# Performance work log

Hardware: AMD Instinct MI355X
Metric: run time of the kernel (lower is better)

## Reference

```python
import jax, jax.numpy as jnp
import numpy as np

B, L, D = 1, 1024, 128
EPS = 1e-5


def setup_inputs() -> dict:
    key = jax.random.key(0)
    ks = jax.random.split(key, 10)
    s = 1.0 / np.sqrt(D)
    return {
        "x": jax.random.normal(ks[0], (B, L, D), dtype=jnp.float32),
        "mask": jax.random.randint(ks[1], (B, L, L), 0, 2, dtype=jnp.int32),
        # JCrossOutProduct.l : Linear(D, D)
        "Wl": jax.random.uniform(ks[2], (D, D), jnp.float32, -s, s),
        "bl": jax.random.uniform(ks[3], (D,), jnp.float32, -s, s),
        # JCrossOutProduct.lo : Linear(D, D)
        "Wlo": jax.random.uniform(ks[4], (D, D), jnp.float32, -s, s),
        "blo": jax.random.uniform(ks[5], (D,), jnp.float32, -s, s),
        # JResCOPAttn.l : Linear(D, D)
        "Wl2": jax.random.uniform(ks[6], (D, D), jnp.float32, -s, s),
        "bl2": jax.random.uniform(ks[7], (D,), jnp.float32, -s, s),
        # LayerNorm(D)
        "gamma": jnp.ones((D,), jnp.float32),
        "beta": jnp.zeros((D,), jnp.float32),
    }


def reference(x, mask, Wl, bl, Wlo, blo, Wl2, bl2, gamma, beta):
    # a = self.cop.l(x) : [B, L, D]
    a = x @ Wl.T + bl
    # outer product kept per-channel: [B, L, L, D]
    outer = jnp.einsum('blc,bmc->blmc', a, a)
    # self.cop.lo over last dim: [B, L, L, D]
    tm = outer @ Wlo.T + blo
    # masked_fill(mask.unsqueeze(-1) == 0, 0.0)
    tm = tm * (mask[..., None] != 0).astype(tm.dtype)
    # tx = self.l(x)
    tx = x @ Wl2.T + bl2
    # per-channel attention-like contraction: out[b,c,d] = sum_a tm[b,c,a,d] * tx[b,a,d]
    y = x + jnp.einsum('bcad,bad->bcd', tm, tx)
    # shadow (eval): Dropout=identity, activator 'none'=identity, LayerNorm(D)
    mu = jnp.mean(y, axis=-1, keepdims=True)
    var = jnp.mean(jnp.square(y - mu), axis=-1, keepdims=True)
    return (y - mu) * jax.lax.rsqrt(var + EPS) * gamma + beta
```

## Files before the change

### kernel.cpp

```cpp
#include <hip/hip_runtime.h>
#include <hip/hip_fp16.h>


typedef _Float16 f16x8 __attribute__((ext_vector_type(8)));
typedef float    f32x4 __attribute__((ext_vector_type(4)));
typedef unsigned int       u32;
typedef unsigned long long u64;

#define LL   1024
#define DD   128
#define EPSV 1e-5f

__global__ __launch_bounds__(256) void prep_kernel(
    const float* __restrict__ x,  const float* __restrict__ Wl,
    const float* __restrict__ bl, const float* __restrict__ Wlo,
    const float* __restrict__ Wl2,const float* __restrict__ bl2,
    _Float16* __restrict__ a_h, float* __restrict__ tx_out,
    _Float16* __restrict__ wh)
{
    __shared__ float xs[16*128];
    __shared__ float wsh[64*129];
    const int t  = threadIdx.x;
    const int bx = blockIdx.x;
    const int by = blockIdx.y;
    const int l0 = by*16;

    #pragma unroll
    for (int i = 0; i < 8; ++i) { int f = i*256 + t; xs[f] = x[l0*DD + f]; }
    const float* Wsrc = ((bx < 2) ? Wl : Wl2) + (bx & 1)*64*DD;
    #pragma unroll
    for (int i = 0; i < 32; ++i) {
        int f = i*256 + t; int r = f >> 7, k = f & 127;
        wsh[r*129 + k] = Wsrc[f];
    }
    __syncthreads();

    const int col  = t & 63;
    const int lsub = t >> 6;
    const float4* X4 = (const float4*)xs;
    float acc0 = 0.f, acc1 = 0.f, acc2 = 0.f, acc3 = 0.f;
    #pragma unroll
    for (int k4 = 0; k4 < 32; ++k4) {
        const float* wp = wsh + col*129 + k4*4;
        float4 wv = {wp[0], wp[1], wp[2], wp[3]};
        float4 x0 = X4[(lsub*4+0)*32 + k4];
        float4 x1 = X4[(lsub*4+1)*32 + k4];
        float4 x2 = X4[(lsub*4+2)*32 + k4];
        float4 x3 = X4[(lsub*4+3)*32 + k4];
        acc0 += wv.x*x0.x + wv.y*x0.y + wv.z*x0.z + wv.w*x0.w;
        acc1 += wv.x*x1.x + wv.y*x1.y + wv.z*x1.z + wv.w*x1.w;
        acc2 += wv.x*x2.x + wv.y*x2.y + wv.z*x2.z + wv.w*x2.w;
        acc3 += wv.x*x3.x + wv.y*x3.y + wv.z*x3.z + wv.w*x3.w;
    }
    const int colg = (bx & 1)*64 + col;
    const float bv = ((bx < 2) ? bl : bl2)[colg];
    if (bx < 2) {
        a_h[(l0+lsub*4+0)*DD + colg] = (_Float16)(acc0 + bv);
        a_h[(l0+lsub*4+1)*DD + colg] = (_Float16)(acc1 + bv);
        a_h[(l0+lsub*4+2)*DD + colg] = (_Float16)(acc2 + bv);
        a_h[(l0+lsub*4+3)*DD + colg] = (_Float16)(acc3 + bv);
    } else {
        tx_out[(l0+lsub*4+0)*DD + colg] = acc0 + bv;
        tx_out[(l0+lsub*4+1)*DD + colg] = acc1 + bv;
        tx_out[(l0+lsub*4+2)*DD + colg] = acc2 + bv;
        tx_out[(l0+lsub*4+3)*DD + colg] = acc3 + bv;
    }

    const int gid = (by*4 + bx)*256 + t;
    if (gid < DD*DD) wh[gid] = (_Float16)Wlo[gid];
}

#define COMPUTE(MI, AM, TV)                                                   \
  do {                                                                        \
    f16x8 ah_[4];                                                             \
    _Pragma("unroll")                                                         \
    for (int k_ = 0; k_ < 4; ++k_) ah_[k_] = al[k_] * (AM)[k_];               \
    f32x4 c_[4];                                                              \
    _Pragma("unroll")                                                         \
    for (int nf_ = 0; nf_ < 4; ++nf_)                                         \
      c_[nf_] = f32x4{blov[nf_], blov[nf_], blov[nf_], blov[nf_]};            \
    _Pragma("unroll")                                                         \
    for (int k_ = 0; k_ < 4; ++k_) {                                          \
      c_[0] = __builtin_amdgcn_mfma_f32_16x16x32_f16(ah_[k_], bh[0][k_], c_[0],0,0,0); \
      c_[1] = __builtin_amdgcn_mfma_f32_16x16x32_f16(ah_[k_], bh[1][k_], c_[1],0,0,0); \
      c_[2] = __builtin_amdgcn_mfma_f32_16x16x32_f16(ah_[k_], bh[2][k_], c_[2],0,0,0); \
      c_[3] = __builtin_amdgcn_mfma_f32_16x16x32_f16(ah_[k_], bh[3][k_], c_[3],0,0,0); \
    }                                                                         \
    _Pragma("unroll")                                                         \
    for (int r_ = 0; r_ < 4; ++r_) {                                          \
      const bool on_ = ((wmb[r_] >> (MI)) & 1ull) != 0;                       \
      _Pragma("unroll")                                                       \
      for (int nf_ = 0; nf_ < 4; ++nf_)                                       \
        y[nf_][r_] = fmaf(on_ ? (TV)[nf_] : 0.0f, c_[nf_][r_], y[nf_][r_]);   \
    }                                                                         \
  } while (0)

__global__ __launch_bounds__(256, 2) void heavy_kernel(
    const _Float16* __restrict__ a_h, const float* __restrict__ tx,
    const _Float16* __restrict__ wh,  const int* __restrict__ mask,
    const float* __restrict__ blo,    float* __restrict__ part)
{
    __shared__ __align__(16) _Float16 ash[64*DD];
    __shared__ __align__(4)  _Float16 txt[DD*66];
    __shared__ u64 mbits[32];
    const int t     = threadIdx.x;
    const int lane  = t & 63, w = t >> 6;
    const int chunk = blockIdx.x;
    const int ltile = blockIdx.y;
    const int l0 = ltile*32, m0 = chunk*64;

    {
        const float4* s4 = (const float4*)(a_h + m0*DD);
        float4* d4 = (float4*)ash;
        #pragma unroll
        for (int i = 0; i < 4; ++i) d4[i*256 + t] = s4[i*256 + t];
    }
    {
        #pragma unroll
        for (int i = 0; i < 8; ++i) {
            int idx = i*256 + t;
            int m = idx >> 5, dg = idx & 31;
            float4 v = *(const float4*)(tx + (m0+m)*DD + dg*4);
            txt[(dg*4+0)*66 + m] = (_Float16)v.x;
            txt[(dg*4+1)*66 + m] = (_Float16)v.y;
            txt[(dg*4+2)*66 + m] = (_Float16)v.z;
            txt[(dg*4+3)*66 + m] = (_Float16)v.w;
        }
    }
    {
        #pragma unroll
        for (int i = 0; i < 8; ++i) {
            int idx = i*256 + t;
            int row = idx >> 6, mcol = idx & 63;
            u64 b = __ballot(mask[(l0 + row)*LL + m0 + mcol] != 0);
            if ((t & 63) == 0) mbits[row] = b;
        }
    }
    __syncthreads();

    const int grp = lane >> 4, ln = lane & 15;
    const int wl = w >> 1, wd = w & 1;
    const int lbase = l0 + wl*16;
    const int dbase = wd*64;

    f16x8 bh[4][4];
    #pragma unroll
    for (int nf = 0; nf < 4; ++nf)
        #pragma unroll
        for (int k = 0; k < 4; ++k)
            bh[nf][k] = *(const f16x8*)(wh + (dbase + nf*16 + ln)*DD + k*32 + grp*8);

    f16x8 al[4];
    #pragma unroll
    for (int k = 0; k < 4; ++k)
        al[k] = *(const f16x8*)(a_h + (lbase + ln)*DD + k*32 + grp*8);

    float blov[4];
    #pragma unroll
    for (int nf = 0; nf < 4; ++nf) blov[nf] = blo[dbase + nf*16 + ln];

    const int lrow0 = wl*16 + grp*4;
    u64 wmb[4];
    #pragma unroll
    for (int r = 0; r < 4; ++r) wmb[r] = mbits[lrow0 + r];

    f32x4 y[4] = {{0,0,0,0},{0,0,0,0},{0,0,0,0},{0,0,0,0}};

    f16x8 amA[4], amB[4];
    float tvA[4], tvB[4], tvC[4], tvD[4];
    #pragma unroll
    for (int k = 0; k < 4; ++k)
        amA[k] = *(const f16x8*)(ash + 0*DD + k*32 + grp*8);
    #pragma unroll
    for (int nf = 0; nf < 4; ++nf) {
        float2 f2 = __half22float2(*(const __half2*)(txt + (dbase + nf*16 + ln)*66));
        tvA[nf] = f2.x; tvB[nf] = f2.y;
    }

    for (int ms = 0; ms < 62; ms += 2) {
        #pragma unroll
        for (int k = 0; k < 4; ++k)
            amB[k] = *(const f16x8*)(ash + (ms+1)*DD + k*32 + grp*8);
        #pragma unroll
        for (int nf = 0; nf < 4; ++nf) {
            float2 f2 = __half22float2(
                *(const __half2*)(txt + (dbase + nf*16 + ln)*66 + ms + 2));
            tvC[nf] = f2.x; tvD[nf] = f2.y;
        }
        COMPUTE(ms, amA, tvA);
        #pragma unroll
        for (int k = 0; k < 4; ++k)
            amA[k] = *(const f16x8*)(ash + (ms+2)*DD + k*32 + grp*8);
        COMPUTE(ms+1, amB, tvB);
        #pragma unroll
        for (int nf = 0; nf < 4; ++nf) { tvA[nf] = tvC[nf]; tvB[nf] = tvD[nf]; }
    }
    {
        #pragma unroll
        for (int k = 0; k < 4; ++k)
            amB[k] = *(const f16x8*)(ash + 63*DD + k*32 + grp*8);
        COMPUTE(62, amA, tvA);
        COMPUTE(63, amB, tvB);
    }

    float* dst = part + (size_t)chunk*(LL*DD);
    const int mrow0 = lbase + grp*4;
    #pragma unroll
    for (int nf = 0; nf < 4; ++nf)
        #pragma unroll
        for (int r = 0; r < 4; ++r)
            dst[(mrow0 + r)*DD + dbase + nf*16 + ln] = y[nf][r];
}

__global__ __launch_bounds__(128) void finish_kernel(
    const float* __restrict__ x, const float* __restrict__ part,
    const float* __restrict__ gamma, const float* __restrict__ beta,
    float* __restrict__ out)
{
    const int l = blockIdx.x, t = threadIdx.x;
    float v = x[l*DD + t];
    #pragma unroll
    for (int ch = 0; ch < 16; ++ch)
        v += part[((size_t)ch*LL + l)*DD + t];

    float s = v, s2 = v*v;
    #pragma unroll
    for (int o = 32; o > 0; o >>= 1) {
        s  += __shfl_xor(s, o);
        s2 += __shfl_xor(s2, o);
    }
    __shared__ float red[4];
    if ((t & 63) == 0) { red[(t>>6)*2+0] = s; red[(t>>6)*2+1] = s2; }
    __syncthreads();
    const float S  = red[0] + red[2];
    const float S2 = red[1] + red[3];
    const float mu  = S * (1.0f/128.0f);
    const float var = S2 * (1.0f/128.0f) - mu*mu;
    const float inv = rsqrtf(var + EPSV);
    out[l*DD + t] = (v - mu)*inv*gamma[t] + beta[t];
}

extern "C" void kernel_launch(void* const* d_in, const int* in_sizes, int n_in,
                              void* d_out, int out_size, void* d_ws, size_t ws_size,
                              hipStream_t stream)
{
    (void)in_sizes; (void)n_in; (void)out_size; (void)ws_size;
    const float* x     = (const float*)d_in[0];
    const int*   mask  = (const int*)  d_in[1];
    const float* Wl    = (const float*)d_in[2];
    const float* bl    = (const float*)d_in[3];
    const float* Wlo   = (const float*)d_in[4];
    const float* blo   = (const float*)d_in[5];
    const float* Wl2   = (const float*)d_in[6];
    const float* bl2   = (const float*)d_in[7];
    const float* gamma = (const float*)d_in[8];
    const float* beta  = (const float*)d_in[9];
    float* out = (float*)d_out;

    char* ws = (char*)d_ws;
    _Float16* a_h  = (_Float16*)(ws);
    float*    tx_b = (float*)   (ws + (256u<<10));
    _Float16* wh   = (_Float16*)(ws + (768u<<10));
    float*    part = (float*)   (ws + (1024u<<10));

    prep_kernel  <<<dim3(4,64),  256, 0, stream>>>(x, Wl, bl, Wlo, Wl2, bl2,
                                                   a_h, tx_b, wh);
    heavy_kernel <<<dim3(16,32), 256, 0, stream>>>(a_h, tx_b, wh, mask, blo, part);
    finish_kernel<<<1024, 128, 0, stream>>>(x, part, gamma, beta, out);
}
```

Measured before the change: 118.2 us.

## Halve heavy-kernel m-chunk to 32, double grid, store partials in fp16

The heavy kernel now handles 32 m-columns per block instead of 64, so the grid doubles to 1024 blocks and more CUs are occupied. Mask bits fit in 32-bit words, and the shared-memory tiles shrink. Partial sums are written as fp16 instead of fp32, which keeps partial-buffer traffic near its old size even though the finish kernel now reduces 32 chunks. The costs are lower accuracy in the fp16 partial sums, more per-block setup (weights and a-rows reloaded in each block), and a longer reduction loop.

```diff
diff --git a/kernel.cpp b/kernel.cpp
--- a/kernel.cpp
+++ b/kernel.cpp
@@ -9,6 +9,8 @@
 
 #define LL   1024
 #define DD   128
+#define MCH  32
+#define TPAD 34
 #define EPSV 1e-5f
 
 __global__ __launch_bounds__(256) void prep_kernel(
@@ -88,7 +90,7 @@
     }                                                                         \
     _Pragma("unroll")                                                         \
     for (int r_ = 0; r_ < 4; ++r_) {                                          \
-      const bool on_ = ((wmb[r_] >> (MI)) & 1ull) != 0;                       \
+      const bool on_ = ((wmb[r_] >> (MI)) & 1u) != 0;                         \
       _Pragma("unroll")                                                       \
       for (int nf_ = 0; nf_ < 4; ++nf_)                                       \
         y[nf_][r_] = fmaf(on_ ? (TV)[nf_] : 0.0f, c_[nf_][r_], y[nf_][r_]);   \
@@ -98,42 +100,43 @@
 __global__ __launch_bounds__(256, 2) void heavy_kernel(
     const _Float16* __restrict__ a_h, const float* __restrict__ tx,
     const _Float16* __restrict__ wh,  const int* __restrict__ mask,
-    const float* __restrict__ blo,    float* __restrict__ part)
-{
-    __shared__ __align__(16) _Float16 ash[64*DD];
-    __shared__ __align__(4)  _Float16 txt[DD*66];
-    __shared__ u64 mbits[32];
+    const float* __restrict__ blo,    _Float16* __restrict__ part)
+{
+    __shared__ __align__(16) _Float16 ash[MCH*DD];
+    __shared__ __align__(4)  _Float16 txt[DD*TPAD];
+    __shared__ u32 mbits[32];
     const int t     = threadIdx.x;
     const int lane  = t & 63, w = t >> 6;
     const int chunk = blockIdx.x;
     const int ltile = blockIdx.y;
-    const int l0 = ltile*32, m0 = chunk*64;
+    const int l0 = ltile*32, m0 = chunk*MCH;
 
     {
         const float4* s4 = (const float4*)(a_h + m0*DD);
         float4* d4 = (float4*)ash;
         #pragma unroll
-        for (int i = 0; i < 4; ++i) d4[i*256 + t] = s4[i*256 + t];
-    }
-    {
-        #pragma unroll
-        for (int i = 0; i < 8; ++i) {
+        for (int i = 0; i < 2; ++i) d4[i*256 + t] = s4[i*256 + t];
+    }
+    {
+        #pragma unroll
+        for (int i = 0; i < 4; ++i) {
             int idx = i*256 + t;
             int m = idx >> 5, dg = idx & 31;
             float4 v = *(const float4*)(tx + (m0+m)*DD + dg*4);
-            txt[(dg*4+0)*66 + m] = (_Float16)v.x;
-            txt[(dg*4+1)*66 + m] = (_Float16)v.y;
-            txt[(dg*4+2)*66 + m] = (_Float16)v.z;
-            txt[(dg*4+3)*66 + m] = (_Float16)v.w;
-        }
-    }
-    {
-        #pragma unroll
-        for (int i = 0; i < 8; ++i) {
+            txt[(dg*4+0)*TPAD + m] = (_Float16)v.x;
+            txt[(dg*4+1)*TPAD + m] = (_Float16)v.y;
+            txt[(dg*4+2)*TPAD + m] = (_Float16)v.z;
+            txt[(dg*4+3)*TPAD + m] = (_Float16)v.w;
+        }
+    }
+    {
+        #pragma unroll
+        for (int i = 0; i < 4; ++i) {
             int idx = i*256 + t;
-            int row = idx >> 6, mcol = idx & 63;
+            int row = idx >> 5, mcol = idx & 31;
             u64 b = __ballot(mask[(l0 + row)*LL + m0 + mcol] != 0);
-            if ((t & 63) == 0) mbits[row] = b;
+            if (lane == 0)  mbits[row]     = (u32)b;
+            if (lane == 32) mbits[row]     = (u32)(b >> 32);
         }
     }
     __syncthreads();
@@ -160,68 +163,67 @@
     for (int nf = 0; nf < 4; ++nf) blov[nf] = blo[dbase + nf*16 + ln];
 
     const int lrow0 = wl*16 + grp*4;
-    u64 wmb[4];
+    u32 wmb[4];
     #pragma unroll
     for (int r = 0; r < 4; ++r) wmb[r] = mbits[lrow0 + r];
 
     f32x4 y[4] = {{0,0,0,0},{0,0,0,0},{0,0,0,0},{0,0,0,0}};
 
     f16x8 amA[4], amB[4];
-    float tvA[4], tvB[4], tvC[4], tvD[4];
+    float tvA[4], tvB[4];
     #pragma unroll
     for (int k = 0; k < 4; ++k)
         amA[k] = *(const f16x8*)(ash + 0*DD + k*32 + grp*8);
-    #pragma unroll
-    for (int nf = 0; nf < 4; ++nf) {
-        float2 f2 = __half22float2(*(const __half2*)(txt + (dbase + nf*16 + ln)*66));
-        tvA[nf] = f2.x; tvB[nf] = f2.y;
-    }
-
-    for (int ms = 0; ms < 62; ms += 2) {
+
+    for (int ms = 0; ms < 30; ms += 2) {
         #pragma unroll
         for (int k = 0; k < 4; ++k)
             amB[k] = *(const f16x8*)(ash + (ms+1)*DD + k*32 + grp*8);
         #pragma unroll
         for (int nf = 0; nf < 4; ++nf) {
             float2 f2 = __half22float2(
-                *(const __half2*)(txt + (dbase + nf*16 + ln)*66 + ms + 2));
-            tvC[nf] = f2.x; tvD[nf] = f2.y;
+                *(const __half2*)(txt + (dbase + nf*16 + ln)*TPAD + ms));
+            tvA[nf] = f2.x; tvB[nf] = f2.y;
         }
         COMPUTE(ms, amA, tvA);
         #pragma unroll
         for (int k = 0; k < 4; ++k)
             amA[k] = *(const f16x8*)(ash + (ms+2)*DD + k*32 + grp*8);
         COMPUTE(ms+1, amB, tvB);
-        #pragma unroll
-        for (int nf = 0; nf < 4; ++nf) { tvA[nf] = tvC[nf]; tvB[nf] = tvD[nf]; }
-    }
-    {
-        #pragma unroll
-        for (int k = 0; k < 4; ++k)
-            amB[k] = *(const f16x8*)(ash + 63*DD + k*32 + grp*8);
-        COMPUTE(62, amA, tvA);
-        COMPUTE(63, amB, tvB);
-    }
-
-    float* dst = part + (size_t)chunk*(LL*DD);
+    }
+    {
+        #pragma unroll
+        for (int k = 0; k < 4; ++k)
+            amB[k] = *(const f16x8*)(ash + 31*DD + k*32 + grp*8);
+        #pragma unroll
+        for (int nf = 0; nf < 4; ++nf) {
+            float2 f2 = __half22float2(
+                *(const __half2*)(txt + (dbase + nf*16 + ln)*TPAD + 30));
+            tvA[nf] = f2.x; tvB[nf] = f2.y;
+        }
+        COMPUTE(30, amA, tvA);
+        COMPUTE(31, amB, tvB);
+    }
+
+    _Float16* dst = part + (size_t)chunk*(LL*DD);
     const int mrow0 = lbase + grp*4;
     #pragma unroll
     for (int nf = 0; nf < 4; ++nf)
         #pragma unroll
         for (int r = 0; r < 4; ++r)
-            dst[(mrow0 + r)*DD + dbase + nf*16 + ln] = y[nf][r];
+            dst[(mrow0 + r)*DD + dbase + nf*16 + ln] = (_Float16)y[nf][r];
 }
 
 __global__ __launch_bounds__(128) void finish_kernel(
-    const float* __restrict__ x, const float* __restrict__ part,
+    const float* __restrict__ x, const _Float16* __restrict__ part,
     const float* __restrict__ gamma, const float* __restrict__ beta,
     float* __restrict__ out)
 {
     const int l = blockIdx.x, t = threadIdx.x;
     float v = x[l*DD + t];
     #pragma unroll
-    for (int ch = 0; ch < 16; ++ch)
-        v += part[((size_t)ch*LL + l)*DD + t];
+    for (int ch = 0; ch < 32; ++ch)
+        v += (float)part[((size_t)ch*LL + l)*DD + t];
 
     float s = v, s2 = v*v;
     #pragma unroll
@@ -261,10 +263,10 @@
     _Float16* a_h  = (_Float16*)(ws);
     float*    tx_b = (float*)   (ws + (256u<<10));
     _Float16* wh   = (_Float16*)(ws + (768u<<10));
-    float*    part = (float*)   (ws + (1024u<<10));
+    _Float16* part = (_Float16*)(ws + (1024u<<10));
 
     prep_kernel  <<<dim3(4,64),  256, 0, stream>>>(x, Wl, bl, Wlo, Wl2, bl2,
                                                    a_h, tx_b, wh);
-    heavy_kernel <<<dim3(16,32), 256, 0, stream>>>(a_h, tx_b, wh, mask, blo, part);
+    heavy_kernel <<<dim3(32,32), 256, 0, stream>>>(a_h, tx_b, wh, mask, blo, part);
     finish_kernel<<<1024, 128, 0, stream>>>(x, part, gamma, beta, out);
 }
```

Measured after the change: 117.4 us. Within noise of the previous version (-0.6%).
